# Performance work log

Hardware: AMD Instinct MI355X
Metric: run time of the kernel (lower is better)

The kernel has to match this reference:

```python
import jax, jax.numpy as jnp
import numpy as np

HIDDEN = 32
SEQ = 1440
IN = 11


def lstm_layer(x, Wih, Whh, bih, bhh):
    # x: (B, T, I); PyTorch gate order i, f, g, o stacked along first dim of W (4H, I)
    B, T, _ = x.shape
    H = Whh.shape[1]
    xg = jnp.einsum('bti,gi->btg', x, Wih) + bih + bhh  # (B, T, 4H) input projections precomputed

    def step(carry, xg_t):
        h, c = carry
        g = xg_t + h @ Whh.T  # (B, 4H)
        i, f, gg, o = jnp.split(g, 4, axis=-1)
        i = jax.nn.sigmoid(i)
        f = jax.nn.sigmoid(f)
        gg = jnp.tanh(gg)
        o = jax.nn.sigmoid(o)
        c = f * c + i * gg
        h = o * jnp.tanh(c)
        return (h, c), h

    h0 = jnp.zeros((B, H), x.dtype)
    (_, _), hs = jax.lax.scan(step, (h0, h0), jnp.swapaxes(xg, 0, 1))  # hs: (T, B, H)
    return jnp.swapaxes(hs, 0, 1)


def setup_inputs() -> dict:
    key = jax.random.key(0)
    ks = jax.random.split(key, 14)
    s = 0.1
    return {
        'x': jax.random.normal(ks[0], (1024, IN, SEQ), dtype=jnp.float32),
        'Wih0': jax.random.normal(ks[1], (4 * HIDDEN, IN), dtype=jnp.float32) * s,
        'Whh0': jax.random.normal(ks[2], (4 * HIDDEN, HIDDEN), dtype=jnp.float32) * s,
        'bih0': jax.random.normal(ks[3], (4 * HIDDEN,), dtype=jnp.float32) * s,
        'bhh0': jax.random.normal(ks[4], (4 * HIDDEN,), dtype=jnp.float32) * s,
        'Wih1': jax.random.normal(ks[5], (4 * HIDDEN, HIDDEN), dtype=jnp.float32) * s,
        'Whh1': jax.random.normal(ks[6], (4 * HIDDEN, HIDDEN), dtype=jnp.float32) * s,
        'bih1': jax.random.normal(ks[7], (4 * HIDDEN,), dtype=jnp.float32) * s,
        'bhh1': jax.random.normal(ks[8], (4 * HIDDEN,), dtype=jnp.float32) * s,
        'fc1_w': jax.random.normal(ks[9], (16, HIDDEN), dtype=jnp.float32) * s,
        'fc1_b': jax.random.normal(ks[10], (16,), dtype=jnp.float32) * s,
        'fc2_w': jax.random.normal(ks[11], (1, 16), dtype=jnp.float32) * s,
        'fc2_b': jax.random.normal(ks[12], (1,), dtype=jnp.float32) * s,
    }


def reference(x, Wih0, Whh0, bih0, bhh0, Wih1, Whh1, bih1, bhh1, fc1_w, fc1_b, fc2_w, fc2_b):
    # x.view(-1, 11, 1440).transpose(1, 2) -> (B, 1440, 11)
    xt = jnp.swapaxes(x.reshape(-1, IN, SEQ), 1, 2)
    h1 = lstm_layer(xt, Wih0, Whh0, bih0, bhh0)
    h2 = lstm_layer(h1, Wih1, Whh1, bih1, bhh1)
    out = h2[:, :SEQ - 1, :]  # out[:, -1440:-1, :] with T=1440 -> steps 0..1438
    out = jnp.tanh(out @ fc1_w.T + fc1_b)
    out = out @ fc2_w.T + fc2_b
    return out.squeeze(-1)  # (B, 1439)
```

## Files before the change

kernel.cpp:

```cpp
#include <hip/hip_runtime.h>

#define H    32
#define SEQ  1440
#define NT   (SEQ - 1)
#define NPH  SEQ
#define INP  11
#define TC   64

#define LOG2E 1.44269504f

__device__ __forceinline__ float rcp_fast(float x)  { return __builtin_amdgcn_rcpf(x); }
__device__ __forceinline__ float exp2_fast(float x) { return __builtin_amdgcn_exp2f(x); }
__device__ __forceinline__ float tanh_f(float x) {
    return fmaf(2.f, rcp_fast(1.f + exp2_fast(x * (-2.f * LOG2E))), -1.f);
}

__global__
__attribute__((amdgpu_flat_work_group_size(256, 256)))
__attribute__((amdgpu_waves_per_eu(2, 4)))
void lstm_fused_kernel(const float* __restrict__ x,
                       const float* __restrict__ Wih0, const float* __restrict__ Whh0,
                       const float* __restrict__ bih0, const float* __restrict__ bhh0,
                       const float* __restrict__ Wih1, const float* __restrict__ Whh1,
                       const float* __restrict__ bih1, const float* __restrict__ bhh1,
                       const float* __restrict__ fc1w_g, const float* __restrict__ fc1b_g,
                       const float* __restrict__ fc2w_g, const float* __restrict__ fc2b_g,
                       float* __restrict__ out)
{
    __shared__ float h0s[2][H];
    __shared__ float h1s[2][H];
    __shared__ float xs[TC][12];
    __shared__ float h1c[2][TC][36];

    const int tid  = threadIdx.x;
    const int half = tid >> 7;
    const int ht   = tid & 127;
    const int l    = ht & 63;
    const int wv   = ht >> 6;
    const int m    = l & 15;
    const int q    = l >> 4;
    const int jj   = wv * 16 + m;
    const int r    = q * 32 + jj;
    const int b    = blockIdx.x;

    const float gsl = ((q == 2) ? 2.f : 1.f) * LOG2E;
    const float am  = (q == 2) ? 2.f : 1.f;
    const float ab  = (q == 2) ? -1.f : 0.f;

    float wA[H], wB[H], bs;
    if (half == 0) {
        #pragma unroll
        for (int k = 0; k < H; ++k) wA[k] = Whh0[r * H + k] * gsl;
        #pragma unroll
        for (int i = 0; i < INP; ++i) wB[i] = Wih0[r * INP + i] * gsl;
        bs = (bih0[r] + bhh0[r]) * gsl;
    } else {
        #pragma unroll
        for (int k = 0; k < H; ++k) {
            wA[k] = Wih1[r * H + k] * gsl;
            wB[k] = Whh1[r * H + k] * gsl;
        }
        bs = (bih1[r] + bhh1[r]) * gsl;
    }

    if (tid < H)          h0s[0][tid] = 0.f;
    else if (tid < 2 * H) h1s[0][tid - H] = 0.f;
    float c = 0.f;

    const float* xb   = x   + (size_t)b * INP * SEQ;
    float*       outb = out + (size_t)b * NT;

    for (int cb = 0; cb < NPH; cb += TC) {
        const int plen = min(TC, NPH - cb);

        {
            const int col = tid & 63;
            const int rw  = tid >> 6;
            if (col < plen) {
                #pragma unroll
                for (int ib = 0; ib < 3; ++ib) {
                    const int row = ib * 4 + rw;
                    xs[col][row] = (row < INP) ? xb[row * SEQ + cb + col] : 0.f;
                }
            }
        }
        __syncthreads();

        for (int pc = 0; pc < plen; ++pc) {
            const int p = cb + pc;
            if (half == 0) {
                if (p < NT) {
                    const float4* xv = (const float4*)xs[pc];
                    const float4* hv = (const float4*)h0s[p & 1];
                    float a0 = bs, a1 = 0.f;
                    float4 x0 = xv[0], x1 = xv[1], x2 = xv[2];
                    a0 = fmaf(wB[0],  x0.x, a0);  a1 = fmaf(wB[1],  x0.y, a1);
                    a0 = fmaf(wB[2],  x0.z, a0);  a1 = fmaf(wB[3],  x0.w, a1);
                    a0 = fmaf(wB[4],  x1.x, a0);  a1 = fmaf(wB[5],  x1.y, a1);
                    a0 = fmaf(wB[6],  x1.z, a0);  a1 = fmaf(wB[7],  x1.w, a1);
                    a0 = fmaf(wB[8],  x2.x, a0);  a1 = fmaf(wB[9],  x2.y, a1);
                    a0 = fmaf(wB[10], x2.z, a0);
                    #pragma unroll
                    for (int kk = 0; kk < 4; ++kk) {
                        float4 ha = hv[kk], hb = hv[kk + 4];
                        a0 = fmaf(wA[4*kk+0],    ha.x, a0);
                        a1 = fmaf(wA[4*kk+1],    ha.y, a1);
                        a0 = fmaf(wA[4*kk+2],    ha.z, a0);
                        a1 = fmaf(wA[4*kk+3],    ha.w, a1);
                        a0 = fmaf(wA[16+4*kk+0], hb.x, a0);
                        a1 = fmaf(wA[16+4*kk+1], hb.y, a1);
                        a0 = fmaf(wA[16+4*kk+2], hb.z, a0);
                        a1 = fmaf(wA[16+4*kk+3], hb.w, a1);
                    }
                    float a   = a0 + a1;
                    float act = fmaf(am, rcp_fast(1.f + exp2_fast(-a)), ab);
                    float gf = __shfl_xor(act, 16);
                    float gg = __shfl_xor(act, 32);
                    float go = __shfl_xor(act, 48);
                    if (q == 0) {
                        c = fmaf(gf, c, act * gg);
                        h0s[(p & 1) ^ 1][jj] = go * tanh_f(c);
                    }
                }
            } else {
                if (p >= 1) {
                    const int s = p - 1;
                    const float4* iv = (const float4*)h0s[p & 1];
                    const float4* hv = (const float4*)h1s[s & 1];
                    float a0 = bs, a1 = 0.f, a2 = 0.f, a3 = 0.f;
                    #pragma unroll
                    for (int kk = 0; kk < 4; ++kk) {
                        float4 ia = iv[kk], ia2 = iv[kk + 4];
                        float4 ha = hv[kk], ha2 = hv[kk + 4];
                        a0 = fmaf(wA[4*kk+0],    ia.x,  a0); a1 = fmaf(wA[4*kk+1],    ia.y,  a1);
                        a2 = fmaf(wA[4*kk+2],    ia.z,  a2); a3 = fmaf(wA[4*kk+3],    ia.w,  a3);
                        a0 = fmaf(wA[16+4*kk+0], ia2.x, a0); a1 = fmaf(wA[16+4*kk+1], ia2.y, a1);
                        a2 = fmaf(wA[16+4*kk+2], ia2.z, a2); a3 = fmaf(wA[16+4*kk+3], ia2.w, a3);
                        a0 = fmaf(wB[4*kk+0],    ha.x,  a0); a1 = fmaf(wB[4*kk+1],    ha.y,  a1);
                        a2 = fmaf(wB[4*kk+2],    ha.z,  a2); a3 = fmaf(wB[4*kk+3],    ha.w,  a3);
                        a0 = fmaf(wB[16+4*kk+0], ha2.x, a0); a1 = fmaf(wB[16+4*kk+1], ha2.y, a1);
                        a2 = fmaf(wB[16+4*kk+2], ha2.z, a2); a3 = fmaf(wB[16+4*kk+3], ha2.w, a3);
                    }
                    float a   = (a0 + a1) + (a2 + a3);
                    float act = fmaf(am, rcp_fast(1.f + exp2_fast(-a)), ab);
                    float gf = __shfl_xor(act, 16);
                    float gg = __shfl_xor(act, 32);
                    float go = __shfl_xor(act, 48);
                    if (q == 0) {
                        c = fmaf(gf, c, act * gg);
                        float hn = go * tanh_f(c);
                        h1s[(s & 1) ^ 1][jj] = hn;
                        h1c[(s >> 6) & 1][s & 63][jj] = hn;
                    }
                }
            }
            __syncthreads();

            if (pc == 0 && cb >= TC) {
                const float (*hc)[36] = h1c[((cb >> 6) - 1) & 1];
                const int u  = tid & 15;
                const int kh = (tid >> 4) & 1;
                const int sl = tid >> 5;
                float fw[16];
                #pragma unroll
                for (int k = 0; k < 16; ++k) fw[k] = fc1w_g[u * H + kh * 16 + k];
                const float fb = fc1b_g[u], f2w = fc2w_g[u], f2b = fc2b_g[0];
                float* outc = outb + (cb - TC);
                #pragma unroll
                for (int rep = 0; rep < 8; ++rep) {
                    const int t2 = sl + 8 * rep;
                    const float4* hv = (const float4*)&hc[t2][kh * 16];
                    float a0 = 0.f, a1 = 0.f;
                    float4 v0 = hv[0], v1 = hv[1], v2 = hv[2], v3 = hv[3];
                    a0 = fmaf(fw[0],  v0.x, a0);  a1 = fmaf(fw[1],  v0.y, a1);
                    a0 = fmaf(fw[2],  v0.z, a0);  a1 = fmaf(fw[3],  v0.w, a1);
                    a0 = fmaf(fw[4],  v1.x, a0);  a1 = fmaf(fw[5],  v1.y, a1);
                    a0 = fmaf(fw[6],  v1.z, a0);  a1 = fmaf(fw[7],  v1.w, a1);
                    a0 = fmaf(fw[8],  v2.x, a0);  a1 = fmaf(fw[9],  v2.y, a1);
                    a0 = fmaf(fw[10], v2.z, a0);  a1 = fmaf(fw[11], v2.w, a1);
                    a0 = fmaf(fw[12], v3.x, a0);  a1 = fmaf(fw[13], v3.y, a1);
                    a0 = fmaf(fw[14], v3.z, a0);  a1 = fmaf(fw[15], v3.w, a1);
                    float y = a0 + a1;
                    y += __shfl_xor(y, 16);
                    float z = tanh_f(y + fb) * f2w;
                    z += __shfl_xor(z, 1);  z += __shfl_xor(z, 2);
                    z += __shfl_xor(z, 4);  z += __shfl_xor(z, 8);
                    if ((tid & 31) == 0) outc[t2] = z + f2b;
                }
            }
        }
    }

    {
        const int tbase = ((NPH - 1) / TC) * TC;
        const int tlen  = NT - tbase;
        const float (*hc)[36] = h1c[(tbase >> 6) & 1];
        const int u  = tid & 15;
        const int kh = (tid >> 4) & 1;
        const int sl = tid >> 5;
        float fw[16];
        #pragma unroll
        for (int k = 0; k < 16; ++k) fw[k] = fc1w_g[u * H + kh * 16 + k];
        const float fb = fc1b_g[u], f2w = fc2w_g[u], f2b = fc2b_g[0];
        float* outc = outb + tbase;
        #pragma unroll
        for (int rep = 0; rep < 8; ++rep) {
            const int t2 = sl + 8 * rep;
            if (t2 < tlen) {
                const float4* hv = (const float4*)&hc[t2][kh * 16];
                float a0 = 0.f, a1 = 0.f;
                float4 v0 = hv[0], v1 = hv[1], v2 = hv[2], v3 = hv[3];
                a0 = fmaf(fw[0],  v0.x, a0);  a1 = fmaf(fw[1],  v0.y, a1);
                a0 = fmaf(fw[2],  v0.z, a0);  a1 = fmaf(fw[3],  v0.w, a1);
                a0 = fmaf(fw[4],  v1.x, a0);  a1 = fmaf(fw[5],  v1.y, a1);
                a0 = fmaf(fw[6],  v1.z, a0);  a1 = fmaf(fw[7],  v1.w, a1);
                a0 = fmaf(fw[8],  v2.x, a0);  a1 = fmaf(fw[9],  v2.y, a1);
                a0 = fmaf(fw[10], v2.z, a0);  a1 = fmaf(fw[11], v2.w, a1);
                a0 = fmaf(fw[12], v3.x, a0);  a1 = fmaf(fw[13], v3.y, a1);
                a0 = fmaf(fw[14], v3.z, a0);  a1 = fmaf(fw[15], v3.w, a1);
                float y = a0 + a1;
                y += __shfl_xor(y, 16);
                float z = tanh_f(y + fb) * f2w;
                z += __shfl_xor(z, 1);  z += __shfl_xor(z, 2);
                z += __shfl_xor(z, 4);  z += __shfl_xor(z, 8);
                if ((tid & 31) == 0) outc[t2] = z + f2b;
            }
        }
    }
}

extern "C" void kernel_launch(void* const* d_in, const int* in_sizes, int n_in,
                              void* d_out, int out_size, void* d_ws, size_t ws_size,
                              hipStream_t stream)
{
    const float* x    = (const float*)d_in[0];
    const float* Wih0 = (const float*)d_in[1];
    const float* Whh0 = (const float*)d_in[2];
    const float* bih0 = (const float*)d_in[3];
    const float* bhh0 = (const float*)d_in[4];
    const float* Wih1 = (const float*)d_in[5];
    const float* Whh1 = (const float*)d_in[6];
    const float* bih1 = (const float*)d_in[7];
    const float* bhh1 = (const float*)d_in[8];
    const float* fc1w = (const float*)d_in[9];
    const float* fc1b = (const float*)d_in[10];
    const float* fc2w = (const float*)d_in[11];
    const float* fc2b = (const float*)d_in[12];
    float* out = (float*)d_out;

    const int B = in_sizes[0] / (INP * SEQ);
    dim3 grid(B), block(256);
    hipLaunchKernelGGL(lstm_fused_kernel, grid, block, 0, stream,
                       x, Wih0, Whh0, bih0, bhh0, Wih1, Whh1, bih1, bhh1,
                       fc1w, fc1b, fc2w, fc2b, out);
}
```

Before: 1.522 ms.

## Process four sequences per block with two sequences per thread

Each block now handles four batch samples with 512 threads: one crew of 256 threads runs layer 0 and the other runs layer 1, and each thread interleaves two sequences so every weight held in registers is used twice per step. Because one __syncthreads now covers more work, the per-step barrier and serial latency are spread over more samples, and the two independent FMA chains give more instruction-level parallelism. In exchange the grid shrinks to B/4 blocks (256 for B=1024) and register pressure rises. It also assumes B is divisible by 4.

```diff
diff --git a/kernel.cpp b/kernel.cpp
--- a/kernel.cpp
+++ b/kernel.cpp
@@ -3,10 +3,8 @@
 #define H    32
 #define SEQ  1440
 #define NT   (SEQ - 1)
-#define NPH  SEQ
 #define INP  11
 #define TC   64
-
 #define LOG2E 1.44269504f
 
 __device__ __forceinline__ float rcp_fast(float x)  { return __builtin_amdgcn_rcpf(x); }
@@ -16,8 +14,7 @@
 }
 
 __global__
-__attribute__((amdgpu_flat_work_group_size(256, 256)))
-__attribute__((amdgpu_waves_per_eu(2, 4)))
+__attribute__((amdgpu_flat_work_group_size(512, 512)))
 void lstm_fused_kernel(const float* __restrict__ x,
                        const float* __restrict__ Wih0, const float* __restrict__ Whh0,
                        const float* __restrict__ bih0, const float* __restrict__ bhh0,
@@ -27,19 +24,19 @@
                        const float* __restrict__ fc2w_g, const float* __restrict__ fc2b_g,
                        float* __restrict__ out)
 {
-    __shared__ float h0s[2][H];
-    __shared__ float h1s[2][H];
-    __shared__ float xs[TC][12];
-    __shared__ float h1c[2][TC][36];
+    __shared__ float h0s[2][4][H];
+    __shared__ float h1s[2][4][H];
+    __shared__ float xs[4][TC][12];
+    __shared__ float h1c[4][2][TC][36];
 
     const int tid  = threadIdx.x;
-    const int half = tid >> 7;
-    const int ht   = tid & 127;
-    const int l    = ht & 63;
-    const int wv   = ht >> 6;
-    const int m    = l & 15;
+    const int crew = tid >> 8;
+    const int sp   = (tid >> 7) & 1;
+    const int sA   = sp * 2, sB = sp * 2 + 1;
+    const int l    = tid & 63;
+    const int w2   = (tid >> 6) & 1;
     const int q    = l >> 4;
-    const int jj   = wv * 16 + m;
+    const int jj   = w2 * 16 + (l & 15);
     const int r    = q * 32 + jj;
     const int b    = blockIdx.x;
 
@@ -48,11 +45,11 @@
     const float ab  = (q == 2) ? -1.f : 0.f;
 
     float wA[H], wB[H], bs;
-    if (half == 0) {
+    if (crew == 0) {
         #pragma unroll
         for (int k = 0; k < H; ++k) wA[k] = Whh0[r * H + k] * gsl;
         #pragma unroll
-        for (int i = 0; i < INP; ++i) wB[i] = Wih0[r * INP + i] * gsl;
+        for (int k = 0; k < H; ++k) wB[k] = (k < INP) ? Wih0[r * INP + k] * gsl : 0.f;
         bs = (bih0[r] + bhh0[r]) * gsl;
     } else {
         #pragma unroll
@@ -63,167 +60,169 @@
         bs = (bih1[r] + bhh1[r]) * gsl;
     }
 
-    if (tid < H)          h0s[0][tid] = 0.f;
-    else if (tid < 2 * H) h1s[0][tid - H] = 0.f;
-    float c = 0.f;
-
-    const float* xb   = x   + (size_t)b * INP * SEQ;
-    float*       outb = out + (size_t)b * NT;
-
-    for (int cb = 0; cb < NPH; cb += TC) {
-        const int plen = min(TC, NPH - cb);
+    if (tid < 128)       h0s[0][tid >> 5][tid & 31] = 0.f;
+    else if (tid < 256)  h1s[0][(tid >> 5) & 3][tid & 31] = 0.f;
+    float c[2] = {0.f, 0.f};
+
+    float* outb = out + (size_t)(4 * b) * NT;
+
+    for (int cb = 0; cb < SEQ; cb += TC) {
+        const int plen = min(TC, SEQ - cb);
 
         {
             const int col = tid & 63;
             const int rw  = tid >> 6;
+            const int ss  = rw >> 1;
+            const int hf  = rw & 1;
             if (col < plen) {
-                #pragma unroll
-                for (int ib = 0; ib < 3; ++ib) {
-                    const int row = ib * 4 + rw;
-                    xs[col][row] = (row < INP) ? xb[row * SEQ + cb + col] : 0.f;
+                const float* xbS = x + (size_t)(4 * b + ss) * INP * SEQ;
+                #pragma unroll
+                for (int ib = 0; ib < 6; ++ib) {
+                    const int row = hf * 6 + ib;
+                    xs[ss][col][row] = (row < INP) ? xbS[row * SEQ + cb + col] : 0.f;
                 }
             }
         }
         __syncthreads();
 
         for (int pc = 0; pc < plen; ++pc) {
-            const int p = cb + pc;
-            if (half == 0) {
+            const int p  = cb + pc;
+            const int pb = p & 1;
+
+            if (crew == 0) {
                 if (p < NT) {
-                    const float4* xv = (const float4*)xs[pc];
-                    const float4* hv = (const float4*)h0s[p & 1];
-                    float a0 = bs, a1 = 0.f;
-                    float4 x0 = xv[0], x1 = xv[1], x2 = xv[2];
-                    a0 = fmaf(wB[0],  x0.x, a0);  a1 = fmaf(wB[1],  x0.y, a1);
-                    a0 = fmaf(wB[2],  x0.z, a0);  a1 = fmaf(wB[3],  x0.w, a1);
-                    a0 = fmaf(wB[4],  x1.x, a0);  a1 = fmaf(wB[5],  x1.y, a1);
-                    a0 = fmaf(wB[6],  x1.z, a0);  a1 = fmaf(wB[7],  x1.w, a1);
-                    a0 = fmaf(wB[8],  x2.x, a0);  a1 = fmaf(wB[9],  x2.y, a1);
-                    a0 = fmaf(wB[10], x2.z, a0);
-                    #pragma unroll
-                    for (int kk = 0; kk < 4; ++kk) {
-                        float4 ha = hv[kk], hb = hv[kk + 4];
-                        a0 = fmaf(wA[4*kk+0],    ha.x, a0);
-                        a1 = fmaf(wA[4*kk+1],    ha.y, a1);
-                        a0 = fmaf(wA[4*kk+2],    ha.z, a0);
-                        a1 = fmaf(wA[4*kk+3],    ha.w, a1);
-                        a0 = fmaf(wA[16+4*kk+0], hb.x, a0);
-                        a1 = fmaf(wA[16+4*kk+1], hb.y, a1);
-                        a0 = fmaf(wA[16+4*kk+2], hb.z, a0);
-                        a1 = fmaf(wA[16+4*kk+3], hb.w, a1);
-                    }
-                    float a   = a0 + a1;
-                    float act = fmaf(am, rcp_fast(1.f + exp2_fast(-a)), ab);
-                    float gf = __shfl_xor(act, 16);
-                    float gg = __shfl_xor(act, 32);
-                    float go = __shfl_xor(act, 48);
+                    const float4* xvA = (const float4*)xs[sA][pc];
+                    const float4* xvB = (const float4*)xs[sB][pc];
+                    const float4* hA  = (const float4*)h0s[pb][sA];
+                    const float4* hB  = (const float4*)h0s[pb][sB];
+                    float aA0 = bs, aA1 = 0.f, aB0 = bs, aB1 = 0.f;
+                    #pragma unroll
+                    for (int kk = 0; kk < 3; ++kk) {
+                        float4 vA = xvA[kk], vB = xvB[kk];
+                        aA0 = fmaf(wB[4*kk+0], vA.x, aA0); aB0 = fmaf(wB[4*kk+0], vB.x, aB0);
+                        aA1 = fmaf(wB[4*kk+1], vA.y, aA1); aB1 = fmaf(wB[4*kk+1], vB.y, aB1);
+                        aA0 = fmaf(wB[4*kk+2], vA.z, aA0); aB0 = fmaf(wB[4*kk+2], vB.z, aB0);
+                        aA1 = fmaf(wB[4*kk+3], vA.w, aA1); aB1 = fmaf(wB[4*kk+3], vB.w, aB1);
+                    }
+                    #pragma unroll
+                    for (int kk = 0; kk < 8; ++kk) {
+                        float4 vA = hA[kk], vB = hB[kk];
+                        aA0 = fmaf(wA[4*kk+0], vA.x, aA0); aB0 = fmaf(wA[4*kk+0], vB.x, aB0);
+                        aA1 = fmaf(wA[4*kk+1], vA.y, aA1); aB1 = fmaf(wA[4*kk+1], vB.y, aB1);
+                        aA0 = fmaf(wA[4*kk+2], vA.z, aA0); aB0 = fmaf(wA[4*kk+2], vB.z, aB0);
+                        aA1 = fmaf(wA[4*kk+3], vA.w, aA1); aB1 = fmaf(wA[4*kk+3], vB.w, aB1);
+                    }
+                    float actA = fmaf(am, rcp_fast(1.f + exp2_fast(-(aA0 + aA1))), ab);
+                    float actB = fmaf(am, rcp_fast(1.f + exp2_fast(-(aB0 + aB1))), ab);
+                    float fA = __shfl_xor(actA, 16), gA = __shfl_xor(actA, 32), oA = __shfl_xor(actA, 48);
+                    float fB = __shfl_xor(actB, 16), gB = __shfl_xor(actB, 32), oB = __shfl_xor(actB, 48);
                     if (q == 0) {
-                        c = fmaf(gf, c, act * gg);
-                        h0s[(p & 1) ^ 1][jj] = go * tanh_f(c);
+                        c[0] = fmaf(fA, c[0], actA * gA);
+                        h0s[pb ^ 1][sA][jj] = oA * tanh_f(c[0]);
+                        c[1] = fmaf(fB, c[1], actB * gB);
+                        h0s[pb ^ 1][sB][jj] = oB * tanh_f(c[1]);
                     }
                 }
             } else {
                 if (p >= 1) {
-                    const int s = p - 1;
-                    const float4* iv = (const float4*)h0s[p & 1];
-                    const float4* hv = (const float4*)h1s[s & 1];
-                    float a0 = bs, a1 = 0.f, a2 = 0.f, a3 = 0.f;
-                    #pragma unroll
-                    for (int kk = 0; kk < 4; ++kk) {
-                        float4 ia = iv[kk], ia2 = iv[kk + 4];
-                        float4 ha = hv[kk], ha2 = hv[kk + 4];
-                        a0 = fmaf(wA[4*kk+0],    ia.x,  a0); a1 = fmaf(wA[4*kk+1],    ia.y,  a1);
-                        a2 = fmaf(wA[4*kk+2],    ia.z,  a2); a3 = fmaf(wA[4*kk+3],    ia.w,  a3);
-                        a0 = fmaf(wA[16+4*kk+0], ia2.x, a0); a1 = fmaf(wA[16+4*kk+1], ia2.y, a1);
-                        a2 = fmaf(wA[16+4*kk+2], ia2.z, a2); a3 = fmaf(wA[16+4*kk+3], ia2.w, a3);
-                        a0 = fmaf(wB[4*kk+0],    ha.x,  a0); a1 = fmaf(wB[4*kk+1],    ha.y,  a1);
-                        a2 = fmaf(wB[4*kk+2],    ha.z,  a2); a3 = fmaf(wB[4*kk+3],    ha.w,  a3);
-                        a0 = fmaf(wB[16+4*kk+0], ha2.x, a0); a1 = fmaf(wB[16+4*kk+1], ha2.y, a1);
-                        a2 = fmaf(wB[16+4*kk+2], ha2.z, a2); a3 = fmaf(wB[16+4*kk+3], ha2.w, a3);
-                    }
-                    float a   = (a0 + a1) + (a2 + a3);
-                    float act = fmaf(am, rcp_fast(1.f + exp2_fast(-a)), ab);
-                    float gf = __shfl_xor(act, 16);
-                    float gg = __shfl_xor(act, 32);
-                    float go = __shfl_xor(act, 48);
+                    const int st = p - 1;
+                    const float4* iA = (const float4*)h0s[pb][sA];
+                    const float4* iB = (const float4*)h0s[pb][sB];
+                    const float4* hA = (const float4*)h1s[pb ^ 1][sA];
+                    const float4* hB = (const float4*)h1s[pb ^ 1][sB];
+                    float aA0 = bs, aA1 = 0.f, aB0 = bs, aB1 = 0.f;
+                    #pragma unroll
+                    for (int kk = 0; kk < 8; ++kk) {
+                        float4 vA = iA[kk], vB = iB[kk];
+                        aA0 = fmaf(wA[4*kk+0], vA.x, aA0); aB0 = fmaf(wA[4*kk+0], vB.x, aB0);
+                        aA1 = fmaf(wA[4*kk+1], vA.y, aA1); aB1 = fmaf(wA[4*kk+1], vB.y, aB1);
+                        aA0 = fmaf(wA[4*kk+2], vA.z, aA0); aB0 = fmaf(wA[4*kk+2], vB.z, aB0);
+                        aA1 = fmaf(wA[4*kk+3], vA.w, aA1); aB1 = fmaf(wA[4*kk+3], vB.w, aB1);
+                    }
+                    #pragma unroll
+                    for (int kk = 0; kk < 8; ++kk) {
+                        float4 vA = hA[kk], vB = hB[kk];
+                        aA0 = fmaf(wB[4*kk+0], vA.x, aA0); aB0 = fmaf(wB[4*kk+0], vB.x, aB0);
+                        aA1 = fmaf(wB[4*kk+1], vA.y, aA1); aB1 = fmaf(wB[4*kk+1], vB.y, aB1);
+                        aA0 = fmaf(wB[4*kk+2], vA.z, aA0); aB0 = fmaf(wB[4*kk+2], vB.z, aB0);
+                        aA1 = fmaf(wB[4*kk+3], vA.w, aA1); aB1 = fmaf(wB[4*kk+3], vB.w, aB1);
+                    }
+                    float actA = fmaf(am, rcp_fast(1.f + exp2_fast(-(aA0 + aA1))), ab);
+                    float actB = fmaf(am, rcp_fast(1.f + exp2_fast(-(aB0 + aB1))), ab);
+                    float fA = __shfl_xor(actA, 16), gA = __shfl_xor(actA, 32), oA = __shfl_xor(actA, 48);
+                    float fB = __shfl_xor(actB, 16), gB = __shfl_xor(actB, 32), oB = __shfl_xor(actB, 48);
                     if (q == 0) {
-                        c = fmaf(gf, c, act * gg);
-                        float hn = go * tanh_f(c);
-                        h1s[(s & 1) ^ 1][jj] = hn;
-                        h1c[(s >> 6) & 1][s & 63][jj] = hn;
+                        const int par = (st >> 6) & 1, tt = st & 63;
+                        c[0] = fmaf(fA, c[0], actA * gA);
+                        float hnA = oA * tanh_f(c[0]);
+                        h1s[pb][sA][jj] = hnA;
+                        h1c[sA][par][tt][jj] = hnA;
+                        c[1] = fmaf(fB, c[1], actB * gB);
+                        float hnB = oB * tanh_f(c[1]);
+                        h1s[pb][sB][jj] = hnB;
+                        h1c[sB][par][tt][jj] = hnB;
                     }
                 }
             }
             __syncthreads();
 
             if (pc == 0 && cb >= TC) {
-                const float (*hc)[36] = h1c[((cb >> 6) - 1) & 1];
-                const int u  = tid & 15;
-                const int kh = (tid >> 4) & 1;
-                const int sl = tid >> 5;
-                float fw[16];
-                #pragma unroll
-                for (int k = 0; k < 16; ++k) fw[k] = fc1w_g[u * H + kh * 16 + k];
-                const float fb = fc1b_g[u], f2w = fc2w_g[u], f2b = fc2b_g[0];
-                float* outc = outb + (cb - TC);
+                const int u   = l & 15;
+                const int gcb = (tid >> 6) * 4 + (l >> 4);
+                const int fs  = gcb >> 3, slot = gcb & 7;
+                const float (*hcp)[36] = h1c[fs][((cb >> 6) - 1) & 1];
+                float fcw[H];
+                #pragma unroll
+                for (int k = 0; k < H; ++k) fcw[k] = fc1w_g[u * H + k];
+                const float fcb = fc1b_g[u], f2w = fc2w_g[u], f2b = fc2b_g[0];
+                float* outc = outb + (size_t)fs * NT + (cb - TC);
                 #pragma unroll
                 for (int rep = 0; rep < 8; ++rep) {
-                    const int t2 = sl + 8 * rep;
-                    const float4* hv = (const float4*)&hc[t2][kh * 16];
-                    float a0 = 0.f, a1 = 0.f;
-                    float4 v0 = hv[0], v1 = hv[1], v2 = hv[2], v3 = hv[3];
-                    a0 = fmaf(fw[0],  v0.x, a0);  a1 = fmaf(fw[1],  v0.y, a1);
-                    a0 = fmaf(fw[2],  v0.z, a0);  a1 = fmaf(fw[3],  v0.w, a1);
-                    a0 = fmaf(fw[4],  v1.x, a0);  a1 = fmaf(fw[5],  v1.y, a1);
-                    a0 = fmaf(fw[6],  v1.z, a0);  a1 = fmaf(fw[7],  v1.w, a1);
-                    a0 = fmaf(fw[8],  v2.x, a0);  a1 = fmaf(fw[9],  v2.y, a1);
-                    a0 = fmaf(fw[10], v2.z, a0);  a1 = fmaf(fw[11], v2.w, a1);
-                    a0 = fmaf(fw[12], v3.x, a0);  a1 = fmaf(fw[13], v3.y, a1);
-                    a0 = fmaf(fw[14], v3.z, a0);  a1 = fmaf(fw[15], v3.w, a1);
-                    float y = a0 + a1;
-                    y += __shfl_xor(y, 16);
-                    float z = tanh_f(y + fb) * f2w;
+                    const int t2 = slot + 8 * rep;
+                    const float4* hv = (const float4*)hcp[t2];
+                    float a0 = fcb, a1 = 0.f;
+                    #pragma unroll
+                    for (int kk = 0; kk < 8; ++kk) {
+                        float4 v = hv[kk];
+                        a0 = fmaf(fcw[4*kk+0], v.x, a0); a1 = fmaf(fcw[4*kk+1], v.y, a1);
+                        a0 = fmaf(fcw[4*kk+2], v.z, a0); a1 = fmaf(fcw[4*kk+3], v.w, a1);
+                    }
+                    float z = tanh_f(a0 + a1) * f2w;
                     z += __shfl_xor(z, 1);  z += __shfl_xor(z, 2);
                     z += __shfl_xor(z, 4);  z += __shfl_xor(z, 8);
-                    if ((tid & 31) == 0) outc[t2] = z + f2b;
+                    if (u == 0) outc[t2] = z + f2b;
                 }
             }
         }
     }
 
     {
-        const int tbase = ((NPH - 1) / TC) * TC;
-        const int tlen  = NT - tbase;
-        const float (*hc)[36] = h1c[(tbase >> 6) & 1];
-        const int u  = tid & 15;
-        const int kh = (tid >> 4) & 1;
-        const int sl = tid >> 5;
-        float fw[16];
-        #pragma unroll
-        for (int k = 0; k < 16; ++k) fw[k] = fc1w_g[u * H + kh * 16 + k];
-        const float fb = fc1b_g[u], f2w = fc2w_g[u], f2b = fc2b_g[0];
-        float* outc = outb + tbase;
+        const int tbase = 1408, tlen = NT - tbase;
+        const int u   = l & 15;
+        const int gcb = (tid >> 6) * 4 + (l >> 4);
+        const int fs  = gcb >> 3, slot = gcb & 7;
+        const float (*hcp)[36] = h1c[fs][(tbase >> 6) & 1];
+        float fcw[H];
+        #pragma unroll
+        for (int k = 0; k < H; ++k) fcw[k] = fc1w_g[u * H + k];
+        const float fcb = fc1b_g[u], f2w = fc2w_g[u], f2b = fc2b_g[0];
+        float* outc = outb + (size_t)fs * NT + tbase;
         #pragma unroll
         for (int rep = 0; rep < 8; ++rep) {
-            const int t2 = sl + 8 * rep;
+            const int t2 = slot + 8 * rep;
             if (t2 < tlen) {
-                const float4* hv = (const float4*)&hc[t2][kh * 16];
-                float a0 = 0.f, a1 = 0.f;
-                float4 v0 = hv[0], v1 = hv[1], v2 = hv[2], v3 = hv[3];
-                a0 = fmaf(fw[0],  v0.x, a0);  a1 = fmaf(fw[1],  v0.y, a1);
-                a0 = fmaf(fw[2],  v0.z, a0);  a1 = fmaf(fw[3],  v0.w, a1);
-                a0 = fmaf(fw[4],  v1.x, a0);  a1 = fmaf(fw[5],  v1.y, a1);
-                a0 = fmaf(fw[6],  v1.z, a0);  a1 = fmaf(fw[7],  v1.w, a1);
-                a0 = fmaf(fw[8],  v2.x, a0);  a1 = fmaf(fw[9],  v2.y, a1);
-                a0 = fmaf(fw[10], v2.z, a0);  a1 = fmaf(fw[11], v2.w, a1);
-                a0 = fmaf(fw[12], v3.x, a0);  a1 = fmaf(fw[13], v3.y, a1);
-                a0 = fmaf(fw[14], v3.z, a0);  a1 = fmaf(fw[15], v3.w, a1);
-                float y = a0 + a1;
-                y += __shfl_xor(y, 16);
-                float z = tanh_f(y + fb) * f2w;
+                const float4* hv = (const float4*)hcp[t2];
+                float a0 = fcb, a1 = 0.f;
+                #pragma unroll
+                for (int kk = 0; kk < 8; ++kk) {
+                    float4 v = hv[kk];
+                    a0 = fmaf(fcw[4*kk+0], v.x, a0); a1 = fmaf(fcw[4*kk+1], v.y, a1);
+                    a0 = fmaf(fcw[4*kk+2], v.z, a0); a1 = fmaf(fcw[4*kk+3], v.w, a1);
+                }
+                float z = tanh_f(a0 + a1) * f2w;
                 z += __shfl_xor(z, 1);  z += __shfl_xor(z, 2);
                 z += __shfl_xor(z, 4);  z += __shfl_xor(z, 8);
-                if ((tid & 31) == 0) outc[t2] = z + f2b;
+                if (u == 0) outc[t2] = z + f2b;
             }
         }
     }
@@ -249,7 +248,7 @@
     float* out = (float*)d_out;
 
     const int B = in_sizes[0] / (INP * SEQ);
-    dim3 grid(B), block(256);
+    dim3 grid(B / 4), block(512);
     hipLaunchKernelGGL(lstm_fused_kernel, grid, block, 0, stream,
                        x, Wih0, Whh0, bih0, bhh0, Wih1, Whh1, bih1, bhh1,
                        fc1w, fc1b, fc2w, fc2b, out);
```

Measured after the change: 1.573 ms. +3.4%, slower.
